# Optimization experiments

Hardware: AMD Instinct MI355X
Metric: run time of the kernel (lower is better)

Reference implementation:

```python
import jax, jax.numpy as jnp
import numpy as np

DIM = 512
HEADS = 16
KS = 5  # side_dwconv


def setup_inputs() -> dict:
    key = jax.random.key(0)
    ks = jax.random.split(key, 6)
    B, H, W = 8, 32, 32
    x = jax.random.normal(ks[0], (B, H, W, DIM), dtype=jnp.float32)
    # qkv linear (no bias): torch Linear weight [3C, C]
    w_qkv = jax.random.normal(ks[1], (3 * DIM, DIM), dtype=jnp.float32) * (1.0 / np.sqrt(DIM))
    # output projection
    w_proj = jax.random.normal(ks[2], (DIM, DIM), dtype=jnp.float32) * (1.0 / np.sqrt(DIM))
    b_proj = jax.random.normal(ks[3], (DIM,), dtype=jnp.float32) * 0.01
    # depthwise conv kernel: torch Conv2d(groups=dim) weight [C, 1, k, k]
    w_lepe = jax.random.normal(ks[4], (DIM, 1, KS, KS), dtype=jnp.float32) * (1.0 / KS)
    b_lepe = jax.random.normal(ks[5], (DIM,), dtype=jnp.float32) * 0.01
    return {"x": x, "w_qkv": w_qkv, "w_proj": w_proj, "b_proj": b_proj,
            "w_lepe": w_lepe, "b_lepe": b_lepe}


def _depthwise_conv(x_nchw, w, b):
    # x: [B, C, H, W], w: [C, 1, k, k] (OIHW with feature_group_count=C)
    out = jax.lax.conv_general_dilated(
        x_nchw, w,
        window_strides=(1, 1),
        padding=[(KS // 2, KS // 2), (KS // 2, KS // 2)],
        dimension_numbers=("NCHW", "OIHW", "NCHW"),
        feature_group_count=x_nchw.shape[1],
    )
    return out + b[None, :, None, None]


def reference(x, w_qkv, w_proj, b_proj, w_lepe, b_lepe):
    B, H, W, C = x.shape
    N = H * W
    hd = C // HEADS
    scale = hd ** (-0.5)

    xt = x.reshape(B, N, C)  # n (h w) c

    qkv = xt @ w_qkv.T  # [B, N, 3C]
    qkv = qkv.reshape(B, N, 3, HEADS, hd).transpose(2, 0, 3, 1, 4)  # [3, B, h, N, d]
    q, k, v = qkv[0], qkv[1], qkv[2]

    # LePE depthwise conv positional encoding
    lepe = _depthwise_conv(xt.reshape(B, H, W, C).transpose(0, 3, 1, 2), w_lepe, b_lepe)
    lepe = lepe.transpose(0, 2, 3, 1).reshape(B, N, C)

    attn = jnp.einsum("bhnd,bhmd->bhnm", q, k) * scale
    attn = jax.nn.softmax(attn, axis=-1)
    out = jnp.einsum("bhnm,bhmd->bhnd", attn, v)
    out = out.transpose(0, 2, 1, 3).reshape(B, N, C)

    out = out + lepe
    out = out @ w_proj.T + b_proj
    return out.reshape(B, H, W, C)
```

## Files before the change

kernel.cpp:

```cpp
#include <hip/hip_runtime.h>
#include <hip/hip_bf16.h>

typedef unsigned int u32;
typedef unsigned short u16;
typedef __attribute__((ext_vector_type(8))) short bfrag;
typedef __attribute__((ext_vector_type(4))) float ffrag;

__device__ __forceinline__ float bf_lo(u32 w) { u32 v = w << 16; return __builtin_bit_cast(float, v); }
__device__ __forceinline__ float bf_hi(u32 w) { u32 v = w & 0xFFFF0000u; return __builtin_bit_cast(float, v); }
__device__ __forceinline__ u16 f2bf_bits(float f) {
  u32 x = __builtin_bit_cast(u32, f);
  x += 0x7FFFu + ((x >> 16) & 1u);
  return (u16)(x >> 16);
}
__device__ __forceinline__ u32 pack2f(float a, float b) {
  __hip_bfloat162 h = __float22bfloat162_rn(float2{a, b});
  u32 r;
  __builtin_memcpy(&r, &h, 4);
  return r;
}
__device__ __forceinline__ u32 bfadd2f(u32 a, u32 b) {
  return pack2f(bf_lo(a) + bf_lo(b), bf_hi(a) + bf_hi(b));
}
__device__ __forceinline__ float fast_exp2(float x) {
#if __has_builtin(__builtin_amdgcn_exp2f)
  return __builtin_amdgcn_exp2f(x);
#else
  return __expf(x * 0.6931471805599453f);
#endif
}

__global__ __launch_bounds__(256) void qkv_gemm(const float* __restrict__ X,
                                                const float* __restrict__ W,
                                                u16* __restrict__ qb,
                                                u16* __restrict__ kb,
                                                u16* __restrict__ vb) {
  __shared__ u16 As[128][40];
  __shared__ u16 Bs[128][40];
  const int tid = threadIdx.x;
  const int lane = tid & 63;
  const int w = tid >> 6;
  const int wr = w >> 1, wc = w & 1;
  const int lrow = lane & 15, quad = lane >> 4;
  const int bm0 = blockIdx.x * 128;
  const int bn0 = blockIdx.y * 128;
  const int lr = tid >> 1;
  const int lc = (tid & 1) * 16;

  ffrag acc[4][4];
#pragma unroll
  for (int i = 0; i < 4; i++)
#pragma unroll
    for (int j = 0; j < 4; j++) acc[i][j] = (ffrag){0.f, 0.f, 0.f, 0.f};

  for (int k0 = 0; k0 < 512; k0 += 32) {
    const float4* ap = (const float4*)(X + (bm0 + lr) * 512 + k0 + lc);
    const float4* bp = (const float4*)(W + (bn0 + lr) * 512 + k0 + lc);
    float4 a0 = ap[0], a1 = ap[1], a2 = ap[2], a3 = ap[3];
    float4 b0 = bp[0], b1 = bp[1], b2 = bp[2], b3 = bp[3];
    __syncthreads();
    u32* as = (u32*)(&As[lr][lc]);
    u32* bs = (u32*)(&Bs[lr][lc]);
    as[0] = pack2f(a0.x, a0.y); as[1] = pack2f(a0.z, a0.w);
    as[2] = pack2f(a1.x, a1.y); as[3] = pack2f(a1.z, a1.w);
    as[4] = pack2f(a2.x, a2.y); as[5] = pack2f(a2.z, a2.w);
    as[6] = pack2f(a3.x, a3.y); as[7] = pack2f(a3.z, a3.w);
    bs[0] = pack2f(b0.x, b0.y); bs[1] = pack2f(b0.z, b0.w);
    bs[2] = pack2f(b1.x, b1.y); bs[3] = pack2f(b1.z, b1.w);
    bs[4] = pack2f(b2.x, b2.y); bs[5] = pack2f(b2.z, b2.w);
    bs[6] = pack2f(b3.x, b3.y); bs[7] = pack2f(b3.z, b3.w);
    __syncthreads();
    bfrag af[4], bf[4];
#pragma unroll
    for (int i = 0; i < 4; i++) af[i] = *(const bfrag*)(&As[wr * 64 + i * 16 + lrow][quad * 8]);
#pragma unroll
    for (int j = 0; j < 4; j++) bf[j] = *(const bfrag*)(&Bs[wc * 64 + j * 16 + lrow][quad * 8]);
#pragma unroll
    for (int i = 0; i < 4; i++)
#pragma unroll
      for (int j = 0; j < 4; j++)
        acc[i][j] = __builtin_amdgcn_mfma_f32_16x16x32_bf16(af[i], bf[j], acc[i][j], 0, 0, 0);
  }

#pragma unroll
  for (int i = 0; i < 4; i++)
#pragma unroll
    for (int j = 0; j < 4; j++) {
      int jj = bn0 + wc * 64 + j * 16 + lrow;
      int which = jj >> 9, rem = jj & 511;
      int h = rem >> 5, d = rem & 31;
      u16* dst = (which == 0) ? qb : (which == 1) ? kb : vb;
#pragma unroll
      for (int r = 0; r < 4; r++) {
        int m = bm0 + wr * 64 + i * 16 + quad * 4 + r;
        int pair = ((m >> 10) << 4) + h;
        int n = m & 1023;
        dst[(pair * 1024 + n) * 32 + d] = f2bf_bits(acc[i][j][r]);
      }
    }
}

__global__ __launch_bounds__(256) void lepe_conv(const float* __restrict__ X,
                                                 const float* __restrict__ Wl,
                                                 const float* __restrict__ bl,
                                                 u16* __restrict__ out) {
  __shared__ float Wls[512 * 25];
  const int tid = threadIdx.x;
  const int c = tid * 2;
  const int y = blockIdx.x;
  const int b = blockIdx.y;
  const int x0 = blockIdx.z * 16;

  {
    const float2* src = (const float2*)Wl;
    float2* dst = (float2*)Wls;
#pragma unroll
    for (int i = 0; i < 25; i++) dst[tid + i * 256] = src[tid + i * 256];
  }
  __syncthreads();

  float w0[25], w1[25];
#pragma unroll
  for (int t = 0; t < 25; t++) {
    w0[t] = Wls[c * 25 + t];
    w1[t] = Wls[(c + 1) * 25 + t];
  }
  const float2 bias = *(const float2*)(bl + c);

  const float* rowp[5];
  bool rowv[5];
#pragma unroll
  for (int r = 0; r < 5; r++) {
    int yy = y + r - 2;
    rowv[r] = (yy >= 0) && (yy < 32);
    rowp[r] = X + ((b * 32 + (rowv[r] ? yy : 0)) * 32) * 512 + c;
  }

  float2 win[5][5];
#pragma unroll
  for (int rel = -2; rel <= 1; rel++) {
    const int slot = ((rel % 5) + 5) % 5;
    const int xcol = x0 + rel;
    const bool xv = (xcol >= 0) && (xcol < 32);
#pragma unroll
    for (int r = 0; r < 5; r++)
      win[r][slot] = (xv && rowv[r]) ? *(const float2*)(rowp[r] + xcol * 512)
                                     : float2{0.f, 0.f};
  }

#pragma unroll
  for (int xi = 0; xi < 16; xi++) {
    {
      const int slot = (xi + 2) % 5;
      const int xcol = x0 + xi + 2;
      const bool xv = (xcol < 32);
#pragma unroll
      for (int r = 0; r < 5; r++)
        win[r][slot] = (xv && rowv[r]) ? *(const float2*)(rowp[r] + xcol * 512)
                                       : float2{0.f, 0.f};
    }
    float a0 = bias.x, a1 = bias.y;
#pragma unroll
    for (int ky = 0; ky < 5; ky++)
#pragma unroll
      for (int kx = 0; kx < 5; kx++) {
        const int rel = xi - 2 + kx;
        const int slot = ((rel % 5) + 5) % 5;
        const float2 v = win[ky][slot];
        const int t = ky * 5 + kx;
        a0 = fmaf(v.x, w0[t], a0);
        a1 = fmaf(v.y, w1[t], a1);
      }
    const int sp = (b * 32 + y) * 32 + x0 + xi;
    *(u32*)(out + sp * 512 + c) = pack2f(a0, a1);
  }
}

__global__ __launch_bounds__(512, 4) void attn_mfma(const u16* __restrict__ qb,
                                                    const u16* __restrict__ kb,
                                                    const u16* __restrict__ vb,
                                                    u16* __restrict__ ao) {
  __shared__ u32 Vt[32][132];
  __shared__ u32 Ps[8][16][20];
  const int tid = threadIdx.x, lane = tid & 63, w = tid >> 6;
  const int quad = lane >> 4, m16 = lane & 15;
  const int pair = blockIdx.x >> 2;
  const int quarter = blockIdx.x & 3;
  const int b = pair >> 4, h = pair & 15;

  const int wq0 = quarter * 256 + w * 32;
  bfrag qf[2];
#pragma unroll
  for (int i = 0; i < 2; i++) {
    int row = wq0 + i * 16 + m16;
    qf[i] = *(const bfrag*)(qb + (pair * 1024 + row) * 32 + quad * 8);
  }

  const float SC2 = 0.25503448540239605f;
  const float SHIFT2 = 11.541560327111707f;
  const u16* kbase = kb + pair * 32768;
  const u16* vbase = vb + pair * 32768;

  bfrag onesf;
#pragma unroll
  for (int e = 0; e < 8; e++) onesf[e] = (short)0x3F80;

  ffrag oacc[2][2], sacc[2];
#pragma unroll
  for (int i = 0; i < 2; i++) {
    oacc[i][0] = (ffrag){0.f, 0.f, 0.f, 0.f};
    oacc[i][1] = (ffrag){0.f, 0.f, 0.f, 0.f};
    sacc[i]    = (ffrag){0.f, 0.f, 0.f, 0.f};
  }

  bfrag kf0n = *(const bfrag*)(kbase + (m16) * 32 + quad * 8);
  bfrag kf1n = *(const bfrag*)(kbase + (16 + m16) * 32 + quad * 8);

  for (int jc = 0; jc < 1024; jc += 256) {
    __syncthreads();
    {
      int task = tid;
      int pp = task & 127;
      int q = task >> 7;
      int g = pp >> 4, t = pp & 15;
      int jlo = jc + g * 32 + t;
      uint4 vl = *(const uint4*)(vbase + jlo * 32 + q * 8);
      uint4 vh = *(const uint4*)(vbase + (jlo + 16) * 32 + q * 8);
      u32 lw[4] = {vl.x, vl.y, vl.z, vl.w};
      u32 hw[4] = {vh.x, vh.y, vh.z, vh.w};
#pragma unroll
      for (int e = 0; e < 4; e++) {
        int d0 = q * 8 + e * 2;
        Vt[d0][pp]     = (lw[e] & 0xFFFFu) | (hw[e] << 16);
        Vt[d0 + 1][pp] = (lw[e] >> 16) | (hw[e] & 0xFFFF0000u);
      }
    }
    __syncthreads();

    for (int j0 = 0; j0 < 256; j0 += 32) {
      const int g0 = j0 >> 5;
      bfrag kf0 = kf0n, kf1 = kf1n;
      {
        const int jn = jc + j0 + 32;
        kf0n = *(const bfrag*)(kbase + (jn + m16) * 32 + quad * 8);
        kf1n = *(const bfrag*)(kbase + (jn + 16 + m16) * 32 + quad * 8);
      }
      ffrag s[2][2];
#pragma unroll
      for (int i = 0; i < 2; i++) {
        s[i][0] = __builtin_amdgcn_mfma_f32_16x16x32_bf16(qf[i], kf0, (ffrag){0.f,0.f,0.f,0.f}, 0, 0, 0);
        s[i][1] = __builtin_amdgcn_mfma_f32_16x16x32_bf16(qf[i], kf1, (ffrag){0.f,0.f,0.f,0.f}, 0, 0, 0);
      }
      bfrag vf0 = *(const bfrag*)(&Vt[m16][g0 * 16 + quad * 4]);
      bfrag vf1 = *(const bfrag*)(&Vt[16 + m16][g0 * 16 + quad * 4]);

#pragma unroll
      for (int i = 0; i < 2; i++) {
#pragma unroll
        for (int r = 0; r < 4; r++) {
          float p0 = fast_exp2(fmaf(s[i][0][r], SC2, -SHIFT2));
          float p1 = fast_exp2(fmaf(s[i][1][r], SC2, -SHIFT2));
          Ps[w][quad * 4 + r][m16] =
              (__builtin_bit_cast(u32, p0) >> 16) | (__builtin_bit_cast(u32, p1) & 0xFFFF0000u);
        }
        bfrag pf = *(const bfrag*)(&Ps[w][m16][quad * 4]);
        oacc[i][0] = __builtin_amdgcn_mfma_f32_16x16x32_bf16(pf, vf0, oacc[i][0], 0, 0, 0);
        oacc[i][1] = __builtin_amdgcn_mfma_f32_16x16x32_bf16(pf, vf1, oacc[i][1], 0, 0, 0);
        sacc[i]    = __builtin_amdgcn_mfma_f32_16x16x32_bf16(pf, onesf, sacc[i], 0, 0, 0);
      }
    }
  }

#pragma unroll
  for (int i = 0; i < 2; i++) {
    float inv[4];
#pragma unroll
    for (int r = 0; r < 4; r++) inv[r] = 1.0f / sacc[i][r];
#pragma unroll
    for (int jd = 0; jd < 2; jd++)
#pragma unroll
      for (int r = 0; r < 4; r++) {
        int row = wq0 + i * 16 + quad * 4 + r;
        int col = jd * 16 + m16;
        ao[(b * 1024 + row) * 512 + h * 32 + col] = f2bf_bits(oacc[i][jd][r] * inv[r]);
      }
  }
}

__global__ __launch_bounds__(256) void proj_gemm(const u16* __restrict__ Y1,
                                                 const u16* __restrict__ Y2,
                                                 const float* __restrict__ W,
                                                 const float* __restrict__ bp,
                                                 float* __restrict__ out) {
  __shared__ u16 As[128][40];
  __shared__ u16 Bs[128][40];
  const int tid = threadIdx.x;
  const int lane = tid & 63;
  const int w = tid >> 6;
  const int wr = w >> 1, wc = w & 1;
  const int lrow = lane & 15, quad = lane >> 4;
  const int bm0 = blockIdx.x * 128;
  const int bn0 = blockIdx.y * 128;
  const int lr = tid >> 1;
  const int lc = (tid & 1) * 16;

  ffrag acc[4][4];
#pragma unroll
  for (int i = 0; i < 4; i++)
#pragma unroll
    for (int j = 0; j < 4; j++) acc[i][j] = (ffrag){0.f, 0.f, 0.f, 0.f};

  for (int k0 = 0; k0 < 512; k0 += 32) {
    const u16* y1p = Y1 + (bm0 + lr) * 512 + k0 + lc;
    const u16* y2p = Y2 + (bm0 + lr) * 512 + k0 + lc;
    uint4 a10 = *(const uint4*)(y1p);
    uint4 a11 = *(const uint4*)(y1p + 8);
    uint4 a20 = *(const uint4*)(y2p);
    uint4 a21 = *(const uint4*)(y2p + 8);
    const float4* wp = (const float4*)(W + (bn0 + lr) * 512 + k0 + lc);
    float4 b0 = wp[0], b1 = wp[1], b2 = wp[2], b3 = wp[3];
    uint4 av0, av1;
    av0.x = bfadd2f(a10.x, a20.x); av0.y = bfadd2f(a10.y, a20.y);
    av0.z = bfadd2f(a10.z, a20.z); av0.w = bfadd2f(a10.w, a20.w);
    av1.x = bfadd2f(a11.x, a21.x); av1.y = bfadd2f(a11.y, a21.y);
    av1.z = bfadd2f(a11.z, a21.z); av1.w = bfadd2f(a11.w, a21.w);
    __syncthreads();
    *(uint4*)(&As[lr][lc])     = av0;
    *(uint4*)(&As[lr][lc + 8]) = av1;
    u32* bs = (u32*)(&Bs[lr][lc]);
    bs[0] = pack2f(b0.x, b0.y); bs[1] = pack2f(b0.z, b0.w);
    bs[2] = pack2f(b1.x, b1.y); bs[3] = pack2f(b1.z, b1.w);
    bs[4] = pack2f(b2.x, b2.y); bs[5] = pack2f(b2.z, b2.w);
    bs[6] = pack2f(b3.x, b3.y); bs[7] = pack2f(b3.z, b3.w);
    __syncthreads();
    bfrag af[4], bf[4];
#pragma unroll
    for (int i = 0; i < 4; i++) af[i] = *(const bfrag*)(&As[wr * 64 + i * 16 + lrow][quad * 8]);
#pragma unroll
    for (int j = 0; j < 4; j++) bf[j] = *(const bfrag*)(&Bs[wc * 64 + j * 16 + lrow][quad * 8]);
#pragma unroll
    for (int i = 0; i < 4; i++)
#pragma unroll
      for (int j = 0; j < 4; j++)
        acc[i][j] = __builtin_amdgcn_mfma_f32_16x16x32_bf16(af[i], bf[j], acc[i][j], 0, 0, 0);
  }

#pragma unroll
  for (int i = 0; i < 4; i++)
#pragma unroll
    for (int j = 0; j < 4; j++) {
      int jj = bn0 + wc * 64 + j * 16 + lrow;
      float bias = bp[jj];
#pragma unroll
      for (int r = 0; r < 4; r++) {
        int m = bm0 + wr * 64 + i * 16 + quad * 4 + r;
        out[m * 512 + jj] = acc[i][j][r] + bias;
      }
    }
}

extern "C" void kernel_launch(void* const* d_in, const int* in_sizes, int n_in,
                              void* d_out, int out_size, void* d_ws, size_t ws_size,
                              hipStream_t stream) {
  const float* x      = (const float*)d_in[0];
  const float* w_qkv  = (const float*)d_in[1];
  const float* w_proj = (const float*)d_in[2];
  const float* b_proj = (const float*)d_in[3];
  const float* w_lepe = (const float*)d_in[4];
  const float* b_lepe = (const float*)d_in[5];
  float* out = (float*)d_out;

  char* ws = (char*)d_ws;
  const size_t SEG = 8388608;
  u16* qb = (u16*)(ws + 0 * SEG);
  u16* kb = (u16*)(ws + 1 * SEG);
  u16* vb = (u16*)(ws + 2 * SEG);
  u16* ao = (u16*)(ws + 3 * SEG);
  u16* lp = (u16*)(ws + 4 * SEG);

  hipLaunchKernelGGL(qkv_gemm, dim3(64, 12), dim3(256), 0, stream, x, w_qkv, qb, kb, vb);
  hipLaunchKernelGGL(lepe_conv, dim3(32, 8, 2), dim3(256), 0, stream, x, w_lepe, b_lepe, lp);
  hipLaunchKernelGGL(attn_mfma, dim3(512), dim3(512), 0, stream, qb, kb, vb, ao);
  hipLaunchKernelGGL(proj_gemm, dim3(64, 4), dim3(256), 0, stream, ao, lp, w_proj, b_proj, out);
}
```

Before: 180.7 us.

## Pre-convert inputs to bf16, fuse LePE add into attention, retile proj GEMM

Adds a conversion kernel that turns x, w_qkv and w_proj into bf16 once per call, so the GEMMs load half the bytes and skip repeated in-loop float-to-bf16 packing. The LePE residual is now added in the attention epilogue instead of the projection prologue, and the projection GEMM uses 128x64 tiles to launch twice as many blocks. In exchange there is an extra kernel launch plus a pass over x and the weights, and the attention epilogue does an extra scattered 2-byte load per output element.

```diff
diff --git a/kernel.cpp b/kernel.cpp
--- a/kernel.cpp
+++ b/kernel.cpp
@@ -6,8 +6,7 @@
 typedef __attribute__((ext_vector_type(8))) short bfrag;
 typedef __attribute__((ext_vector_type(4))) float ffrag;
 
-__device__ __forceinline__ float bf_lo(u32 w) { u32 v = w << 16; return __builtin_bit_cast(float, v); }
-__device__ __forceinline__ float bf_hi(u32 w) { u32 v = w & 0xFFFF0000u; return __builtin_bit_cast(float, v); }
+__device__ __forceinline__ float bf2f(u16 h) { u32 v = ((u32)h) << 16; return __builtin_bit_cast(float, v); }
 __device__ __forceinline__ u16 f2bf_bits(float f) {
   u32 x = __builtin_bit_cast(u32, f);
   x += 0x7FFFu + ((x >> 16) & 1u);
@@ -18,9 +17,6 @@
   u32 r;
   __builtin_memcpy(&r, &h, 4);
   return r;
-}
-__device__ __forceinline__ u32 bfadd2f(u32 a, u32 b) {
-  return pack2f(bf_lo(a) + bf_lo(b), bf_hi(a) + bf_hi(b));
 }
 __device__ __forceinline__ float fast_exp2(float x) {
 #if __has_builtin(__builtin_amdgcn_exp2f)
@@ -30,8 +26,30 @@
 #endif
 }
 
-__global__ __launch_bounds__(256) void qkv_gemm(const float* __restrict__ X,
-                                                const float* __restrict__ W,
+__global__ __launch_bounds__(256) void cvt_bf16(const float* __restrict__ X,
+                                                const float* __restrict__ Wq,
+                                                const float* __restrict__ Wp,
+                                                u16* __restrict__ xb,
+                                                u16* __restrict__ wqb,
+                                                u16* __restrict__ wpb) {
+  const int idx = blockIdx.x * 256 + threadIdx.x;
+  const int NX = 1048576;
+  const int NQ = 196608;
+  const float* src;
+  u16* dst;
+  int off;
+  if (idx < NX)            { src = X;  dst = xb;  off = idx; }
+  else if (idx < NX + NQ)  { src = Wq; dst = wqb; off = idx - NX; }
+  else                     { src = Wp; dst = wpb; off = idx - NX - NQ; }
+  float4 v = ((const float4*)src)[off];
+  uint2 r;
+  r.x = pack2f(v.x, v.y);
+  r.y = pack2f(v.z, v.w);
+  ((uint2*)dst)[off] = r;
+}
+
+__global__ __launch_bounds__(256) void qkv_gemm(const u16* __restrict__ Xb,
+                                                const u16* __restrict__ Wqb,
                                                 u16* __restrict__ qb,
                                                 u16* __restrict__ kb,
                                                 u16* __restrict__ vb) {
@@ -54,21 +72,15 @@
     for (int j = 0; j < 4; j++) acc[i][j] = (ffrag){0.f, 0.f, 0.f, 0.f};
 
   for (int k0 = 0; k0 < 512; k0 += 32) {
-    const float4* ap = (const float4*)(X + (bm0 + lr) * 512 + k0 + lc);
-    const float4* bp = (const float4*)(W + (bn0 + lr) * 512 + k0 + lc);
-    float4 a0 = ap[0], a1 = ap[1], a2 = ap[2], a3 = ap[3];
-    float4 b0 = bp[0], b1 = bp[1], b2 = bp[2], b3 = bp[3];
-    __syncthreads();
-    u32* as = (u32*)(&As[lr][lc]);
-    u32* bs = (u32*)(&Bs[lr][lc]);
-    as[0] = pack2f(a0.x, a0.y); as[1] = pack2f(a0.z, a0.w);
-    as[2] = pack2f(a1.x, a1.y); as[3] = pack2f(a1.z, a1.w);
-    as[4] = pack2f(a2.x, a2.y); as[5] = pack2f(a2.z, a2.w);
-    as[6] = pack2f(a3.x, a3.y); as[7] = pack2f(a3.z, a3.w);
-    bs[0] = pack2f(b0.x, b0.y); bs[1] = pack2f(b0.z, b0.w);
-    bs[2] = pack2f(b1.x, b1.y); bs[3] = pack2f(b1.z, b1.w);
-    bs[4] = pack2f(b2.x, b2.y); bs[5] = pack2f(b2.z, b2.w);
-    bs[6] = pack2f(b3.x, b3.y); bs[7] = pack2f(b3.z, b3.w);
+    const uint4* ap = (const uint4*)(Xb + (bm0 + lr) * 512 + k0 + lc);
+    const uint4* bp = (const uint4*)(Wqb + (bn0 + lr) * 512 + k0 + lc);
+    uint4 a0 = ap[0], a1 = ap[1];
+    uint4 b0 = bp[0], b1 = bp[1];
+    __syncthreads();
+    *(uint4*)(&As[lr][lc])     = a0;
+    *(uint4*)(&As[lr][lc + 8]) = a1;
+    *(uint4*)(&Bs[lr][lc])     = b0;
+    *(uint4*)(&Bs[lr][lc + 8]) = b1;
     __syncthreads();
     bfrag af[4], bf[4];
 #pragma unroll
@@ -179,6 +191,7 @@
 __global__ __launch_bounds__(512, 4) void attn_mfma(const u16* __restrict__ qb,
                                                     const u16* __restrict__ kb,
                                                     const u16* __restrict__ vb,
+                                                    const u16* __restrict__ lp,
                                                     u16* __restrict__ ao) {
   __shared__ u32 Vt[32][132];
   __shared__ u32 Ps[8][16][20];
@@ -282,74 +295,63 @@
       for (int r = 0; r < 4; r++) {
         int row = wq0 + i * 16 + quad * 4 + r;
         int col = jd * 16 + m16;
-        ao[(b * 1024 + row) * 512 + h * 32 + col] = f2bf_bits(oacc[i][jd][r] * inv[r]);
-      }
-  }
-}
-
-__global__ __launch_bounds__(256) void proj_gemm(const u16* __restrict__ Y1,
-                                                 const u16* __restrict__ Y2,
-                                                 const float* __restrict__ W,
+        int o = (b * 1024 + row) * 512 + h * 32 + col;
+        float val = fmaf(oacc[i][jd][r], inv[r], bf2f(lp[o]));
+        ao[o] = f2bf_bits(val);
+      }
+  }
+}
+
+__global__ __launch_bounds__(256) void proj_gemm(const u16* __restrict__ Y,
+                                                 const u16* __restrict__ Wpb,
                                                  const float* __restrict__ bp,
                                                  float* __restrict__ out) {
   __shared__ u16 As[128][40];
-  __shared__ u16 Bs[128][40];
+  __shared__ u16 Bs[64][40];
   const int tid = threadIdx.x;
   const int lane = tid & 63;
   const int w = tid >> 6;
   const int wr = w >> 1, wc = w & 1;
   const int lrow = lane & 15, quad = lane >> 4;
   const int bm0 = blockIdx.x * 128;
-  const int bn0 = blockIdx.y * 128;
+  const int bn0 = blockIdx.y * 64;
   const int lr = tid >> 1;
   const int lc = (tid & 1) * 16;
-
-  ffrag acc[4][4];
+  const int br = tid >> 2;
+  const int bc = (tid & 3) * 8;
+
+  ffrag acc[4][2];
 #pragma unroll
   for (int i = 0; i < 4; i++)
 #pragma unroll
-    for (int j = 0; j < 4; j++) acc[i][j] = (ffrag){0.f, 0.f, 0.f, 0.f};
+    for (int j = 0; j < 2; j++) acc[i][j] = (ffrag){0.f, 0.f, 0.f, 0.f};
 
   for (int k0 = 0; k0 < 512; k0 += 32) {
-    const u16* y1p = Y1 + (bm0 + lr) * 512 + k0 + lc;
-    const u16* y2p = Y2 + (bm0 + lr) * 512 + k0 + lc;
-    uint4 a10 = *(const uint4*)(y1p);
-    uint4 a11 = *(const uint4*)(y1p + 8);
-    uint4 a20 = *(const uint4*)(y2p);
-    uint4 a21 = *(const uint4*)(y2p + 8);
-    const float4* wp = (const float4*)(W + (bn0 + lr) * 512 + k0 + lc);
-    float4 b0 = wp[0], b1 = wp[1], b2 = wp[2], b3 = wp[3];
-    uint4 av0, av1;
-    av0.x = bfadd2f(a10.x, a20.x); av0.y = bfadd2f(a10.y, a20.y);
-    av0.z = bfadd2f(a10.z, a20.z); av0.w = bfadd2f(a10.w, a20.w);
-    av1.x = bfadd2f(a11.x, a21.x); av1.y = bfadd2f(a11.y, a21.y);
-    av1.z = bfadd2f(a11.z, a21.z); av1.w = bfadd2f(a11.w, a21.w);
-    __syncthreads();
-    *(uint4*)(&As[lr][lc])     = av0;
-    *(uint4*)(&As[lr][lc + 8]) = av1;
-    u32* bs = (u32*)(&Bs[lr][lc]);
-    bs[0] = pack2f(b0.x, b0.y); bs[1] = pack2f(b0.z, b0.w);
-    bs[2] = pack2f(b1.x, b1.y); bs[3] = pack2f(b1.z, b1.w);
-    bs[4] = pack2f(b2.x, b2.y); bs[5] = pack2f(b2.z, b2.w);
-    bs[6] = pack2f(b3.x, b3.y); bs[7] = pack2f(b3.z, b3.w);
-    __syncthreads();
-    bfrag af[4], bf[4];
+    const uint4* ap = (const uint4*)(Y + (bm0 + lr) * 512 + k0 + lc);
+    uint4 a0 = ap[0], a1 = ap[1];
+    uint4 b0 = *(const uint4*)(Wpb + (bn0 + br) * 512 + k0 + bc);
+    __syncthreads();
+    *(uint4*)(&As[lr][lc])     = a0;
+    *(uint4*)(&As[lr][lc + 8]) = a1;
+    *(uint4*)(&Bs[br][bc])     = b0;
+    __syncthreads();
+    bfrag af[4], bf[2];
 #pragma unroll
     for (int i = 0; i < 4; i++) af[i] = *(const bfrag*)(&As[wr * 64 + i * 16 + lrow][quad * 8]);
 #pragma unroll
-    for (int j = 0; j < 4; j++) bf[j] = *(const bfrag*)(&Bs[wc * 64 + j * 16 + lrow][quad * 8]);
+    for (int j = 0; j < 2; j++) bf[j] = *(const bfrag*)(&Bs[wc * 32 + j * 16 + lrow][quad * 8]);
 #pragma unroll
     for (int i = 0; i < 4; i++)
 #pragma unroll
-      for (int j = 0; j < 4; j++)
+      for (int j = 0; j < 2; j++)
         acc[i][j] = __builtin_amdgcn_mfma_f32_16x16x32_bf16(af[i], bf[j], acc[i][j], 0, 0, 0);
   }
 
 #pragma unroll
   for (int i = 0; i < 4; i++)
 #pragma unroll
-    for (int j = 0; j < 4; j++) {
-      int jj = bn0 + wc * 64 + j * 16 + lrow;
+    for (int j = 0; j < 2; j++) {
+      int jj = bn0 + wc * 32 + j * 16 + lrow;
       float bias = bp[jj];
 #pragma unroll
       for (int r = 0; r < 4; r++) {
@@ -372,14 +374,18 @@
 
   char* ws = (char*)d_ws;
   const size_t SEG = 8388608;
-  u16* qb = (u16*)(ws + 0 * SEG);
-  u16* kb = (u16*)(ws + 1 * SEG);
-  u16* vb = (u16*)(ws + 2 * SEG);
-  u16* ao = (u16*)(ws + 3 * SEG);
-  u16* lp = (u16*)(ws + 4 * SEG);
-
-  hipLaunchKernelGGL(qkv_gemm, dim3(64, 12), dim3(256), 0, stream, x, w_qkv, qb, kb, vb);
+  u16* qb  = (u16*)(ws + 0 * SEG);
+  u16* kb  = (u16*)(ws + 1 * SEG);
+  u16* vb  = (u16*)(ws + 2 * SEG);
+  u16* ao  = (u16*)(ws + 3 * SEG);
+  u16* lp  = (u16*)(ws + 4 * SEG);
+  u16* xb  = (u16*)(ws + 5 * SEG);
+  u16* wqb = (u16*)(ws + 6 * SEG);
+  u16* wpb = (u16*)(ws + 6 * SEG + 1572864);
+
+  hipLaunchKernelGGL(cvt_bf16, dim3(5120), dim3(256), 0, stream, x, w_qkv, w_proj, xb, wqb, wpb);
+  hipLaunchKernelGGL(qkv_gemm, dim3(64, 12), dim3(256), 0, stream, xb, wqb, qb, kb, vb);
   hipLaunchKernelGGL(lepe_conv, dim3(32, 8, 2), dim3(256), 0, stream, x, w_lepe, b_lepe, lp);
-  hipLaunchKernelGGL(attn_mfma, dim3(512), dim3(512), 0, stream, qb, kb, vb, ao);
-  hipLaunchKernelGGL(proj_gemm, dim3(64, 4), dim3(256), 0, stream, ao, lp, w_proj, b_proj, out);
-}
+  hipLaunchKernelGGL(attn_mfma, dim3(512), dim3(512), 0, stream, qb, kb, vb, lp, ao);
+  hipLaunchKernelGGL(proj_gemm, dim3(64, 8), dim3(256), 0, stream, ao, wpb, b_proj, out);
+}
```

Result: faster. 165.7 us (-8.3%).
